# Performance work log

Measured on AMD Instinct MI355X. Metric: run time of the kernel, lower is better.

The kernel has to match this reference:

```python
import jax, jax.numpy as jnp
import numpy as np

B, L, DIN, D, H, NL, DFF = 4, 1024, 64, 512, 8, 3, 2048
DH = D // H
N_RBF = 8
LARGE_NEG, CLAMP = 10000.0, 20.0


def layernorm(x, g, b, eps=1e-5):
    m = x.mean(-1, keepdims=True)
    v = x.var(-1, keepdims=True)
    return (x - m) * jax.lax.rsqrt(v + eps) * g + b


def sinusoidal_pe(length, d):
    pos = np.arange(length, dtype=np.float32)[:, None]
    div = np.exp(np.arange(0, d, 2, dtype=np.float32) * (-np.log(10000.0) / d))
    pe = np.zeros((length, d), dtype=np.float32)
    pe[:, 0::2] = np.sin(pos * div)
    pe[:, 1::2] = np.cos(pos * div)
    return jnp.asarray(pe)


def rbf(v):
    centers = jnp.linspace(0.0, 1.0, N_RBF)
    widths = jnp.full((N_RBF,), 0.2)
    diff = (v[..., None] - centers) / (widths + 1e-6)
    return jnp.exp(-0.5 * diff * diff)


def setup_inputs() -> dict:
    key = jax.random.key(0)
    ks = jax.random.split(key, 40)
    g = lambda k, shape: (jax.random.normal(k, shape) * 0.02).astype(jnp.float32)
    feat_dim = D + 2 + 2 * N_RBF  # base PE + raw(2) + 2 RBFs
    inp = {
        "x": jax.random.normal(ks[0], (B, L, DIN), jnp.float32),
        "lengths": jax.random.randint(ks[1], (B,), L // 2, L + 1),
        "input_delay": jax.random.uniform(ks[2], (B,), jnp.float32),
        "c_local": jax.random.uniform(ks[3], (B, L), jnp.float32).at[:, 0].set(0.0),
        "c_sink": jax.random.uniform(ks[4], (B, L), jnp.float32),
        # input projection
        "in_w": g(ks[5], (D, DIN)), "in_b": jnp.zeros((D,)),
        # delay encoder: Linear(1,D) -> GELU -> Linear(D,D) -> LN
        "de_w1": g(ks[6], (D, 1)), "de_b1": jnp.zeros((D,)),
        "de_w2": g(ks[7], (D, D)), "de_b2": jnp.zeros((D,)),
        "de_ln_g": jnp.ones((D,)), "de_ln_b": jnp.zeros((D,)),
        # corr positional encoding
        "cpe_w": g(ks[8], (D, feat_dim)), "cpe_b": jnp.zeros((D,)),
        "cpe_ln_g": jnp.ones((D,)), "cpe_ln_b": jnp.zeros((D,)),
        "gain": jnp.float32(0.5),
        # bias params
        "alpha": jnp.float32(10.0), "beta": jnp.float32(10.0),
        "floor": jnp.float32(0.1), "gamma": jnp.float32(0.7),
        # per-layer stacks
        "inproj_w": g(ks[9], (NL, 3 * D, D)), "inproj_b": jnp.zeros((NL, 3 * D)),
        "outproj_w": g(ks[10], (NL, D, D)), "outproj_b": jnp.zeros((NL, D)),
        "ln1_g": jnp.ones((NL, D)), "ln1_b": jnp.zeros((NL, D)),
        "ln2_g": jnp.ones((NL, D)), "ln2_b": jnp.zeros((NL, D)),
        "ff_w1": g(ks[11], (NL, DFF, D)), "ff_b1": jnp.zeros((NL, DFF)),
        "ff_w2": g(ks[12], (NL, D, DFF)), "ff_b2": jnp.zeros((NL, D)),
        "out_ln_g": jnp.ones((D,)), "out_ln_b": jnp.zeros((D,)),
    }
    return inp


def _forward(x, input_delay, c_local, c_sink, in_w, in_b, de_w1, de_b1, de_w2, de_b2,
             de_ln_g, de_ln_b, cpe_w, cpe_b, cpe_ln_g, cpe_ln_b, gain, alpha, beta,
             floor, gamma, inproj_w, inproj_b, outproj_w, outproj_b, ln1_g, ln1_b,
             ln2_g, ln2_b, ff_w1, ff_b1, ff_w2, ff_b2, out_ln_g, out_ln_b, lengths):
    Bc, Lc, _ = x.shape
    mask = jnp.arange(Lc)[None, :] >= lengths[:, None]          # [B,L] True=pad

    # input projection
    h = x @ in_w.T + in_b

    # delay feature encoder
    e = input_delay[:, None] @ de_w1.T + de_b1
    e = jax.nn.gelu(e, approximate=False) @ de_w2.T + de_b2
    e = layernorm(e, de_ln_g, de_ln_b)
    h = h + e[:, None, :]

    # corr positional encoding (uses clamped correlations)
    cl = jnp.clip(c_local, 0.0, 1.0)
    cs = jnp.clip(c_sink, 0.0, 1.0)
    pe_base = jnp.broadcast_to(sinusoidal_pe(Lc, D)[None], (Bc, Lc, D))
    z = jnp.concatenate([pe_base, jnp.stack([cl, cs], -1), rbf(cl), rbf(cs)], axis=-1)
    pe = layernorm(z @ cpe_w.T + cpe_b, cpe_ln_g, cpe_ln_b)
    pe = gain * pe
    pe = jnp.where(mask[..., None], 0.0, pe)
    h = h + pe

    # neighbor-correlation attention bias [B,1,L,L] (identical across layers/heads)
    idx = jnp.arange(Lc)
    neigh = jnp.abs(idx[None, :] - idx[:, None]) == 1           # [L,L]
    c_edge = jnp.zeros((Bc, Lc, Lc), x.dtype)
    c_edge = c_edge.at[:, 1:, :-1].set(jnp.broadcast_to(c_local[:, 1:, None], (Bc, Lc - 1, Lc - 1)))
    c_edge = c_edge.at[:, :-1, 1:].set(jnp.broadcast_to(c_local[:, None, 1:], (Bc, Lc - 1, Lc - 1)))
    bias = alpha * jnp.where(neigh[None], c_edge, 0.0)
    bias = jnp.where(mask[:, :, None] | mask[:, None, :], 0.0, bias)

    # sink bias (row 0 only): floor + (1-floor)*(c_sink^gamma)
    c_remap = floor + (1.0 - floor) * jnp.power(cs + 1e-6, gamma)
    sink_row = beta * jnp.where(mask, 0.0, c_remap)             # [B,L]
    attn_bias = bias[:, None].at[:, :, 0, :].add(sink_row[:, None, :])  # [B,1,L,L]

    pad = mask[:, None, None, :].astype(x.dtype)                # [B,1,1,L]
    scale = 1.0 / (DH ** 0.5)

    for i in range(NL):
        hn = layernorm(h, ln1_g[i], ln1_b[i])
        qkv = hn @ inproj_w[i].T + inproj_b[i]                  # [B,L,3D]
        q, k, v = jnp.split(qkv, 3, axis=-1)
        q = q.reshape(Bc, Lc, H, DH).transpose(0, 2, 1, 3)      # [B,H,L,d]
        k = k.reshape(Bc, Lc, H, DH).transpose(0, 2, 1, 3)
        v = v.reshape(Bc, Lc, H, DH).transpose(0, 2, 1, 3)
        scores = jnp.einsum('bhqd,bhkd->bhqk', q, k) * scale + attn_bias
        scores = scores - LARGE_NEG * pad
        scores = scores - scores.max(axis=-1, keepdims=True)
        scores = jnp.clip(scores, -CLAMP, CLAMP)
        attn = jax.nn.softmax(scores, axis=-1)
        o = jnp.einsum('bhqk,bhkd->bhqd', attn, v)
        o = o.transpose(0, 2, 1, 3).reshape(Bc, Lc, D)
        h = h + (o @ outproj_w[i].T + outproj_b[i])
        hn2 = layernorm(h, ln2_g[i], ln2_b[i])
        ff = jax.nn.gelu(hn2 @ ff_w1[i].T + ff_b1[i], approximate=False)
        h = h + (ff @ ff_w2[i].T + ff_b2[i])

    return layernorm(h, out_ln_g, out_ln_b)


def reference(x, lengths, input_delay, c_local, c_sink, in_w, in_b, de_w1, de_b1,
              de_w2, de_b2, de_ln_g, de_ln_b, cpe_w, cpe_b, cpe_ln_g, cpe_ln_b, gain,
              alpha, beta, floor, gamma, inproj_w, inproj_b, outproj_w, outproj_b,
              ln1_g, ln1_b, ln2_g, ln2_b, ff_w1, ff_b1, ff_w2, ff_b2, out_ln_g, out_ln_b):
    return _forward(x, input_delay, c_local, c_sink, in_w, in_b, de_w1, de_b1, de_w2,
                    de_b2, de_ln_g, de_ln_b, cpe_w, cpe_b, cpe_ln_g, cpe_ln_b, gain,
                    alpha, beta, floor, gamma, inproj_w, inproj_b, outproj_w,
                    outproj_b, ln1_g, ln1_b, ln2_g, ln2_b, ff_w1, ff_b1, ff_w2, ff_b2,
                    out_ln_g, out_ln_b, lengths)
```

## Files before the change

### kernel.cpp

```cpp
#include <hip/hip_runtime.h>
#include <math.h>

#define BB 4
#define LL 1024
#define DIN 64
#define DD 512
#define HH 8
#define DH 64
#define NLAYER 3
#define DFF 2048
#define FEAT 530
#define FEATP 576
#define MM 4096

typedef float f32x4 __attribute__((ext_vector_type(4)));
typedef short s16x8 __attribute__((ext_vector_type(8)));

__device__ __forceinline__ unsigned short f2bf(float f) {
    unsigned int u = __float_as_uint(f);
    u += 0x7fffu + ((u >> 16) & 1u);
    return (unsigned short)(u >> 16);
}
__device__ __forceinline__ float bf2f(unsigned short u) {
    return __uint_as_float(((unsigned int)u) << 16);
}
__device__ __forceinline__ float gelu_exact(float x) {
    return 0.5f * x * (1.0f + erff(x * 0.7071067811865475f));
}
__device__ __forceinline__ float wave_reduce_sum(float v) {
    #pragma unroll
    for (int o = 32; o; o >>= 1) v += __shfl_down(v, o);
    return v;
}
__device__ __forceinline__ void gload16(const unsigned short* g, unsigned short* l) {
    __builtin_amdgcn_global_load_lds(
        (const __attribute__((address_space(1))) unsigned int*)g,
        (__attribute__((address_space(3))) unsigned int*)l, 16, 0, 0);
}

__global__ __launch_bounds__(256) void prep_kernel(
    const float* __restrict__ x, const float* __restrict__ inproj_w,
    const float* __restrict__ outproj_w, const float* __restrict__ ff_w1,
    const float* __restrict__ ff_w2, const float* __restrict__ in_w,
    const float* __restrict__ cpe_w,
    unsigned short* __restrict__ x_bf, unsigned short* __restrict__ w_inproj,
    unsigned short* __restrict__ w_outproj, unsigned short* __restrict__ w_ff1,
    unsigned short* __restrict__ w_ff2, unsigned short* __restrict__ w_in,
    unsigned short* __restrict__ w_cpe)
{
    const int N0 = MM * DIN;
    const int N1 = N0 + 3 * 1536 * 512;
    const int N2 = N1 + 3 * 512 * 512;
    const int N3 = N2 + 3 * 2048 * 512;
    const int N4 = N3 + 3 * 512 * 2048;
    const int N5 = N4 + 512 * 64;
    const int N6 = N5 + 512 * FEATP;
    for (int i = blockIdx.x * 256 + threadIdx.x; i < N6; i += gridDim.x * 256) {
        if (i < N0)      x_bf[i]          = f2bf(x[i]);
        else if (i < N1) w_inproj[i - N0] = f2bf(inproj_w[i - N0]);
        else if (i < N2) w_outproj[i - N1]= f2bf(outproj_w[i - N1]);
        else if (i < N3) w_ff1[i - N2]    = f2bf(ff_w1[i - N2]);
        else if (i < N4) w_ff2[i - N3]    = f2bf(ff_w2[i - N3]);
        else if (i < N5) w_in[i - N4]     = f2bf(in_w[i - N4]);
        else {
            int j = i - N5; int r = j / FEATP, c = j - r * FEATP;
            w_cpe[j] = (c < FEAT) ? f2bf(cpe_w[(size_t)r * FEAT + c]) : 0;
        }
    }
}

__global__ __launch_bounds__(256) void build_z_kernel(
    const float* __restrict__ c_local, const float* __restrict__ c_sink,
    const int* __restrict__ lengths,
    const float* __restrict__ beta_p, const float* __restrict__ floor_p,
    const float* __restrict__ gamma_p,
    unsigned short* __restrict__ Z, float* __restrict__ srow)
{
    int row = blockIdx.x;
    int b = row >> 10, l = row & 1023;
    int t = threadIdx.x;
    unsigned short* zr = Z + (size_t)row * FEATP;
    for (int d = t; d < DD; d += 256) {
        int i = d >> 1;
        float dv = expf((float)(2 * i) * (-0.017988946135618352f));
        float ang = (float)l * dv;
        zr[d] = f2bf((d & 1) ? cosf(ang) : sinf(ang));
    }
    if (t < 64) {
        float cl = c_local[(size_t)b * LL + l]; cl = fminf(fmaxf(cl, 0.f), 1.f);
        float cs = c_sink [(size_t)b * LL + l]; cs = fminf(fmaxf(cs, 0.f), 1.f);
        float v = 0.f;
        if (t == 0) v = cl;
        else if (t == 1) v = cs;
        else if (t < 10)  { float c = (float)(t - 2) * (1.0f / 7.0f);  float df = (cl - c) / 0.200001f; v = expf(-0.5f * df * df); }
        else if (t < 18)  { float c = (float)(t - 10) * (1.0f / 7.0f); float df = (cs - c) / 0.200001f; v = expf(-0.5f * df * df); }
        zr[512 + t] = (t < 18) ? f2bf(v) : 0;
        if (t == 32) {
            float sv = (*beta_p) * ((*floor_p) + (1.f - (*floor_p)) * powf(cs + 1e-6f, *gamma_p));
            srow[row] = (l < lengths[b]) ? sv : 0.f;
        }
    }
}

__global__ __launch_bounds__(512) void delay_kernel(
    const float* __restrict__ delay, const float* __restrict__ w1, const float* __restrict__ b1,
    const float* __restrict__ w2, const float* __restrict__ b2,
    const float* __restrict__ lng, const float* __restrict__ lnb,
    float* __restrict__ e)
{
    int b = blockIdx.x;
    int t = threadIdx.x;
    __shared__ float g1[DD];
    __shared__ float red[16];
    float t1 = delay[b] * w1[t] + b1[t];
    g1[t] = gelu_exact(t1);
    __syncthreads();
    const float* wr = w2 + (size_t)t * DD;
    float s = b2[t];
    for (int j = 0; j < DD; j += 4) {
        float4 w4 = *(const float4*)(wr + j);
        s += w4.x * g1[j] + w4.y * g1[j+1] + w4.z * g1[j+2] + w4.w * g1[j+3];
    }
    float rs = wave_reduce_sum(s);
    float rss = wave_reduce_sum(s * s);
    int lane = t & 63, w = t >> 6;
    if (lane == 0) { red[w] = rs; red[8 + w] = rss; }
    __syncthreads();
    float mean = 0.f, msq = 0.f;
    #pragma unroll
    for (int i = 0; i < 8; ++i) { mean += red[i]; msq += red[8 + i]; }
    mean *= (1.0f / DD); msq *= (1.0f / DD);
    float rstd = rsqrtf(msq - mean * mean + 1e-5f);
    e[(size_t)b * DD + t] = (s - mean) * rstd * lng[t] + lnb[t];
}

template<int BM, int BN, int FM, int FN, int WGN, int MODE>
__global__ __launch_bounds__(256) void gemm_t(
    const unsigned short* __restrict__ A, const unsigned short* __restrict__ W,
    const float* __restrict__ bias, const float* __restrict__ resid,
    float* __restrict__ outf, unsigned short* __restrict__ outb,
    int M, int N, int K)
{
    __shared__ __align__(16) unsigned short As[2][BM * 64];
    __shared__ __align__(16) unsigned short Ws[2][BN * 64];
    int bm = blockIdx.y * BM, bn = blockIdx.x * BN;
    int t = threadIdx.x;
    int lane = t & 63, wid = t >> 6;
    int wr = wid / WGN, wc = wid % WGN;
    int l15 = lane & 15, lg = lane >> 4;
    int sr = lane >> 3;
    int sc = ((lane & 7) ^ sr) * 8;
    int ph0 = (lg ^ (l15 & 7)) * 8;
    int ph1 = ((lg + 4) ^ (l15 & 7)) * 8;

    f32x4 acc[FM][FN] = {};
    int nk = K >> 6;

    auto stage = [&](int buf, int ks) {
        int kb = ks * 64;
        #pragma unroll
        for (int i = 0; i < BM / 32; ++i) {
            int row = wid * (BM / 4) + i * 8 + sr;
            gload16(A + (size_t)(bm + row) * K + kb + sc, &As[buf][(wid * (BM / 4) + i * 8) * 64]);
        }
        #pragma unroll
        for (int i = 0; i < BN / 32; ++i) {
            int row = wid * (BN / 4) + i * 8 + sr;
            gload16(W + (size_t)(bn + row) * K + kb + sc, &Ws[buf][(wid * (BN / 4) + i * 8) * 64]);
        }
    };

    stage(0, 0);
    __syncthreads();

    int cur = 0;
    for (int ks = 0; ks < nk; ++ks) {
        if (ks + 1 < nk) stage(cur ^ 1, ks + 1);
        s16x8 af0[FM], af1[FM], wf0[FN], wf1[FN];
        #pragma unroll
        for (int mi = 0; mi < FM; ++mi) {
            int row = wr * FM * 16 + mi * 16 + l15;
            af0[mi] = *(const s16x8*)&As[cur][row * 64 + ph0];
            af1[mi] = *(const s16x8*)&As[cur][row * 64 + ph1];
        }
        #pragma unroll
        for (int ni = 0; ni < FN; ++ni) {
            int row = wc * FN * 16 + ni * 16 + l15;
            wf0[ni] = *(const s16x8*)&Ws[cur][row * 64 + ph0];
            wf1[ni] = *(const s16x8*)&Ws[cur][row * 64 + ph1];
        }
        #pragma unroll
        for (int mi = 0; mi < FM; ++mi)
            #pragma unroll
            for (int ni = 0; ni < FN; ++ni) {
                acc[mi][ni] = __builtin_amdgcn_mfma_f32_16x16x32_bf16(af0[mi], wf0[ni], acc[mi][ni], 0, 0, 0);
                acc[mi][ni] = __builtin_amdgcn_mfma_f32_16x16x32_bf16(af1[mi], wf1[ni], acc[mi][ni], 0, 0, 0);
            }
        __syncthreads();
        cur ^= 1;
    }

    int rbase = (lane >> 4) * 4;
    #pragma unroll
    for (int mi = 0; mi < FM; ++mi) {
        #pragma unroll
        for (int ni = 0; ni < FN; ++ni) {
            int n = bn + wc * FN * 16 + ni * 16 + l15;
            float bzc = (MODE == 4) ? 0.f : bias[n];
            #pragma unroll
            for (int r2 = 0; r2 < 4; ++r2) {
                int m = bm + wr * FM * 16 + mi * 16 + rbase + r2;
                float v = acc[mi][ni][r2] + ((MODE == 4) ? bias[m] : bzc);
                size_t o = (size_t)m * N + n;
                if (MODE == 0)      outf[o] = v;
                else if (MODE == 1) outb[o] = f2bf(v);
                else if (MODE == 2) outf[o] = v + resid[o];
                else if (MODE == 3) outb[o] = f2bf(gelu_exact(v));
                else                outb[o] = f2bf(v);
            }
        }
    }
}

#define SK 72
#define SPB 72
__global__ __launch_bounds__(256) void attn_mfma(
    const unsigned short* __restrict__ qk, const unsigned short* __restrict__ Vt,
    const float* __restrict__ c_local, const float* __restrict__ srow,
    const int* __restrict__ lengths,
    const float* __restrict__ alpha_p,
    unsigned short* __restrict__ o)
{
    __shared__ __align__(16) unsigned short Ks[2][64 * SK];
    __shared__ __align__(16) unsigned short Vts[2][64 * SK];
    __shared__ __align__(16) unsigned short Psb[64 * SPB];

    int id = blockIdx.x;
    int q0 = (id & 15) * 64;
    int hh = (id >> 4) & 7;
    int b  = id >> 7;

    int t  = threadIdx.x;
    int lane = t & 63, w = t >> 6;
    int l15 = lane & 15, lg = lane >> 4;
    int len = lengths[b];
    int nt = (len + 63) >> 6;
    int kt0 = q0 >> 6;
    bool sink_blk = (q0 == 0);
    const float alpha = *alpha_p;

    const unsigned short* qrow = qk + (size_t)(b * LL + q0 + w * 16 + l15) * 1024 + hh * DH;
    s16x8 qf0 = *(const s16x8*)(qrow + lg * 8);
    s16x8 qf1 = *(const s16x8*)(qrow + 32 + lg * 8);
    #pragma unroll
    for (int j = 0; j < 8; ++j) {
        qf0[j] = (short)f2bf(bf2f((unsigned short)qf0[j]) * 0.125f);
        qf1[j] = (short)f2bf(bf2f((unsigned short)qf1[j]) * 0.125f);
    }

    float cm1[4], cp1[4];
    #pragma unroll
    for (int r2 = 0; r2 < 4; ++r2) {
        int qi = q0 + w * 16 + lg * 4 + r2;
        cm1[r2] = 0.f; cp1[r2] = 0.f;
        if (qi >= 1 && qi < len) {
            int src = (qi == 1 || qi == LL - 1) ? qi : qi - 1;
            cm1[r2] = alpha * c_local[(size_t)b * LL + src];
        }
        if (qi + 1 < LL && qi < len)
            cp1[r2] = alpha * c_local[(size_t)b * LL + qi + 1];
    }
    bool need_sink = (sink_blk && w == 0 && lg == 0);

    float m_run[4], l_run[4];
    f32x4 accO[4] = {};
    #pragma unroll
    for (int r2 = 0; r2 < 4; ++r2) { m_run[r2] = -1e30f; l_run[r2] = 0.f; }

    int sr = t >> 3, sc8 = (t & 7) * 8;
    const unsigned short* kbase = qk + (size_t)(b * LL) * 1024 + 512 + hh * DH;
    const unsigned short* vbase = Vt + (size_t)(hh * DH) * MM + b * LL;

    uint4 pk0 = *(const uint4*)(kbase + (size_t)sr * 1024 + sc8);
    uint4 pk1 = *(const uint4*)(kbase + (size_t)(sr + 32) * 1024 + sc8);
    uint4 pv0 = *(const uint4*)(vbase + (size_t)sr * MM + sc8);
    uint4 pv1 = *(const uint4*)(vbase + (size_t)(sr + 32) * MM + sc8);
    *(uint4*)&Ks[0][sr * SK + sc8]         = pk0;
    *(uint4*)&Ks[0][(sr + 32) * SK + sc8]  = pk1;
    *(uint4*)&Vts[0][sr * SK + sc8]        = pv0;
    *(uint4*)&Vts[0][(sr + 32) * SK + sc8] = pv1;
    __syncthreads();

    int cur = 0;
    for (int kt = 0; kt < nt; ++kt) {
        int k0 = kt * 64;
        bool pre = (kt + 1 < nt);
        if (pre) {
            int kn = k0 + 64;
            pk0 = *(const uint4*)(kbase + (size_t)(kn + sr) * 1024 + sc8);
            pk1 = *(const uint4*)(kbase + (size_t)(kn + sr + 32) * 1024 + sc8);
            pv0 = *(const uint4*)(vbase + (size_t)sr * MM + kn + sc8);
            pv1 = *(const uint4*)(vbase + (size_t)(sr + 32) * MM + kn + sc8);
        }

        f32x4 accS[4] = {};
        #pragma unroll
        for (int ct = 0; ct < 4; ++ct) {
            s16x8 kf0 = *(const s16x8*)&Ks[cur][(ct * 16 + l15) * SK + lg * 8];
            s16x8 kf1 = *(const s16x8*)&Ks[cur][(ct * 16 + l15) * SK + 32 + lg * 8];
            accS[ct] = __builtin_amdgcn_mfma_f32_16x16x32_bf16(qf0, kf0, accS[ct], 0, 0, 0);
            accS[ct] = __builtin_amdgcn_mfma_f32_16x16x32_bf16(qf1, kf1, accS[ct], 0, 0, 0);
        }

        float m4[4] = { -1e30f, -1e30f, -1e30f, -1e30f };
        bool slow = sink_blk || (kt >= kt0 - 1 && kt <= kt0 + 1) || (k0 + 64 > len);
        if (!slow) {
            #pragma unroll
            for (int ct = 0; ct < 4; ++ct)
                #pragma unroll
                for (int r2 = 0; r2 < 4; ++r2)
                    m4[r2] = fmaxf(m4[r2], accS[ct][r2]);
        } else if (k0 + 64 <= len) {
            #pragma unroll
            for (int ct = 0; ct < 4; ++ct) {
                int k = k0 + ct * 16 + l15;
                float sink_ct = need_sink ? srow[(size_t)b * LL + k] : 0.f;
                #pragma unroll
                for (int r2 = 0; r2 < 4; ++r2) {
                    int qi = q0 + w * 16 + lg * 4 + r2;
                    float v = accS[ct][r2];
                    if (k == qi - 1) v += cm1[r2];
                    else if (k == qi + 1) v += cp1[r2];
                    if (r2 == 0) v += sink_ct;
                    accS[ct][r2] = v;
                    m4[r2] = fmaxf(m4[r2], v);
                }
            }
        } else {
            #pragma unroll
            for (int ct = 0; ct < 4; ++ct) {
                int k = k0 + ct * 16 + l15;
                bool maskk = (k >= len);
                float sink_ct = need_sink ? srow[(size_t)b * LL + k] : 0.f;
                #pragma unroll
                for (int r2 = 0; r2 < 4; ++r2) {
                    int qi = q0 + w * 16 + lg * 4 + r2;
                    float v = accS[ct][r2];
                    if (k == qi - 1) v += cm1[r2];
                    else if (k == qi + 1 && !maskk) v += cp1[r2];
                    if (r2 == 0) v += sink_ct;
                    if (maskk) v -= 10000.f;
                    accS[ct][r2] = v;
                    m4[r2] = fmaxf(m4[r2], v);
                }
            }
        }

        #pragma unroll
        for (int r2 = 0; r2 < 4; ++r2) {
            #pragma unroll
            for (int msk = 1; msk < 16; msk <<= 1) m4[r2] = fmaxf(m4[r2], __shfl_xor(m4[r2], msk));
            float mnew = fmaxf(m_run[r2], m4[r2]);
            float scl = __expf(m_run[r2] - mnew);
            m_run[r2] = mnew;
            float rowsum = 0.f;
            #pragma unroll
            for (int ct = 0; ct < 4; ++ct) {
                float p = __expf(accS[ct][r2] - mnew);
                rowsum += p;
                Psb[(w * 16 + lg * 4 + r2) * SPB + ct * 16 + l15] = f2bf(p);
            }
            #pragma unroll
            for (int msk = 1; msk < 16; msk <<= 1) rowsum += __shfl_xor(rowsum, msk);
            l_run[r2] = l_run[r2] * scl + rowsum;
            #pragma unroll
            for (int dt = 0; dt < 4; ++dt) accO[dt][r2] *= scl;
        }

        #pragma unroll
        for (int kk = 0; kk < 2; ++kk) {
            s16x8 pf = *(const s16x8*)&Psb[(w * 16 + l15) * SPB + kk * 32 + lg * 8];
            #pragma unroll
            for (int dt = 0; dt < 4; ++dt) {
                s16x8 vf = *(const s16x8*)&Vts[cur][(dt * 16 + l15) * SK + kk * 32 + lg * 8];
                accO[dt] = __builtin_amdgcn_mfma_f32_16x16x32_bf16(pf, vf, accO[dt], 0, 0, 0);
            }
        }

        if (pre) {
            int nxt = cur ^ 1;
            *(uint4*)&Ks[nxt][sr * SK + sc8]         = pk0;
            *(uint4*)&Ks[nxt][(sr + 32) * SK + sc8]  = pk1;
            *(uint4*)&Vts[nxt][sr * SK + sc8]        = pv0;
            *(uint4*)&Vts[nxt][(sr + 32) * SK + sc8] = pv1;
        }
        __syncthreads();
        cur ^= 1;
    }

    #pragma unroll
    for (int r2 = 0; r2 < 4; ++r2) {
        float inv = 1.f / l_run[r2];
        int qi = q0 + w * 16 + lg * 4 + r2;
        #pragma unroll
        for (int dt = 0; dt < 4; ++dt)
            o[(size_t)(b * LL + qi) * DD + hh * DH + dt * 16 + l15] = f2bf(accO[dt][r2] * inv);
    }
}

__global__ __launch_bounds__(256) void embed_ep_kernel(
    const float* __restrict__ cpe_pre, const float* __restrict__ e,
    const int* __restrict__ lengths,
    const float* __restrict__ cpe_g, const float* __restrict__ cpe_lb,
    const float* __restrict__ gain_p, float* __restrict__ h)
{
    int row = blockIdx.x;
    int b = row >> 10, l = row & 1023;
    int t = threadIdx.x;
    __shared__ float red[16];
    const float* cp = cpe_pre + (size_t)row * DD;
    float v0 = cp[t], v1 = cp[t + 256];
    float s = v0 + v1, ss = v0 * v0 + v1 * v1;
    float rs = wave_reduce_sum(s), rss = wave_reduce_sum(ss);
    int lane = t & 63, w = t >> 6;
    if (lane == 0) { red[w] = rs; red[8 + w] = rss; }
    __syncthreads();
    float mean = 0.f, msq = 0.f;
    #pragma unroll
    for (int i = 0; i < 4; ++i) { mean += red[i]; msq += red[8 + i]; }
    mean *= (1.0f / DD); msq *= (1.0f / DD);
    float rstd = rsqrtf(msq - mean * mean + 1e-5f);
    bool maskp = (l >= lengths[b]);
    float gain = *gain_p;
    float pe0 = maskp ? 0.f : gain * ((v0 - mean) * rstd * cpe_g[t] + cpe_lb[t]);
    float pe1 = maskp ? 0.f : gain * ((v1 - mean) * rstd * cpe_g[t + 256] + cpe_lb[t + 256]);
    h[(size_t)row * DD + t]       += e[(size_t)b * DD + t] + pe0;
    h[(size_t)row * DD + t + 256] += e[(size_t)b * DD + t + 256] + pe1;
}

__global__ __launch_bounds__(256) void ln_kernel(
    const float* __restrict__ in, float* __restrict__ out,
    const float* __restrict__ g, const float* __restrict__ bta)
{
    int row = blockIdx.x; int t = threadIdx.x;
    __shared__ float red[16];
    const float* xr = in + (size_t)row * DD;
    float2 v = ((const float2*)xr)[t];
    float s = v.x + v.y, ss = v.x * v.x + v.y * v.y;
    float rs = wave_reduce_sum(s), rss = wave_reduce_sum(ss);
    int lane = t & 63, w = t >> 6;
    if (lane == 0) { red[w] = rs; red[8 + w] = rss; }
    __syncthreads();
    float mean = 0.f, msq = 0.f;
    #pragma unroll
    for (int i = 0; i < 4; ++i) { mean += red[i]; msq += red[8 + i]; }
    mean *= (1.0f / DD); msq *= (1.0f / DD);
    float rstd = rsqrtf(msq - mean * mean + 1e-5f);
    float2 gg = ((const float2*)g)[t], bb = ((const float2*)bta)[t];
    float2 o;
    o.x = (v.x - mean) * rstd * gg.x + bb.x;
    o.y = (v.y - mean) * rstd * gg.y + bb.y;
    ((float2*)(out + (size_t)row * DD))[t] = o;
}

__global__ __launch_bounds__(256) void ln_bf16_kernel(
    const float* __restrict__ in, unsigned short* __restrict__ out,
    const float* __restrict__ g, const float* __restrict__ bta)
{
    int row = blockIdx.x; int t = threadIdx.x;
    __shared__ float red[16];
    const float* xr = in + (size_t)row * DD;
    float2 v = ((const float2*)xr)[t];
    float s = v.x + v.y, ss = v.x * v.x + v.y * v.y;
    float rs = wave_reduce_sum(s), rss = wave_reduce_sum(ss);
    int lane = t & 63, w = t >> 6;
    if (lane == 0) { red[w] = rs; red[8 + w] = rss; }
    __syncthreads();
    float mean = 0.f, msq = 0.f;
    #pragma unroll
    for (int i = 0; i < 4; ++i) { mean += red[i]; msq += red[8 + i]; }
    mean *= (1.0f / DD); msq *= (1.0f / DD);
    float rstd = rsqrtf(msq - mean * mean + 1e-5f);
    float2 gg = ((const float2*)g)[t], bb = ((const float2*)bta)[t];
    ushort2 o;
    o.x = f2bf((v.x - mean) * rstd * gg.x + bb.x);
    o.y = f2bf((v.y - mean) * rstd * gg.y + bb.y);
    ((ushort2*)(out + (size_t)row * DD))[t] = o;
}

extern "C" void kernel_launch(void* const* d_in, const int* in_sizes, int n_in,
                              void* d_out, int out_size, void* d_ws, size_t ws_size,
                              hipStream_t stream)
{
    const float* x          = (const float*)d_in[0];
    const int*   lengths    = (const int*)  d_in[1];
    const float* input_delay= (const float*)d_in[2];
    const float* c_local    = (const float*)d_in[3];
    const float* c_sink     = (const float*)d_in[4];
    const float* in_w       = (const float*)d_in[5];
    const float* in_b       = (const float*)d_in[6];
    const float* de_w1      = (const float*)d_in[7];
    const float* de_b1      = (const float*)d_in[8];
    const float* de_w2      = (const float*)d_in[9];
    const float* de_b2      = (const float*)d_in[10];
    const float* de_ln_g    = (const float*)d_in[11];
    const float* de_ln_b    = (const float*)d_in[12];
    const float* cpe_w      = (const float*)d_in[13];
    const float* cpe_b      = (const float*)d_in[14];
    const float* cpe_ln_g   = (const float*)d_in[15];
    const float* cpe_ln_b   = (const float*)d_in[16];
    const float* gain       = (const float*)d_in[17];
    const float* alpha      = (const float*)d_in[18];
    const float* beta       = (const float*)d_in[19];
    const float* floorp     = (const float*)d_in[20];
    const float* gammap     = (const float*)d_in[21];
    const float* inproj_w   = (const float*)d_in[22];
    const float* inproj_b   = (const float*)d_in[23];
    const float* outproj_w  = (const float*)d_in[24];
    const float* outproj_b  = (const float*)d_in[25];
    const float* ln1_g      = (const float*)d_in[26];
    const float* ln1_b      = (const float*)d_in[27];
    const float* ln2_g      = (const float*)d_in[28];
    const float* ln2_b      = (const float*)d_in[29];
    const float* ff_w1      = (const float*)d_in[30];
    const float* ff_b1      = (const float*)d_in[31];
    const float* ff_w2      = (const float*)d_in[32];
    const float* ff_b2      = (const float*)d_in[33];
    const float* out_ln_g   = (const float*)d_in[34];
    const float* out_ln_b   = (const float*)d_in[35];

    char* base = (char*)d_ws;
    float* h            = (float*)base;
    unsigned short* act1 = (unsigned short*)(base + 8u*1024*1024);
    char* bigb          = base + 12u*1024*1024;
    unsigned short* qkb  = (unsigned short*)bigb;
    unsigned short* vtb  = (unsigned short*)(bigb + 12u*1024*1024);
    unsigned short* ffb  = (unsigned short*)bigb;
    unsigned short* Zb   = (unsigned short*)bigb;
    unsigned short* x_bf = (unsigned short*)(bigb + 5u*1024*1024);
    float* cpe_pre       = (float*)(bigb + 8u*1024*1024);
    unsigned short* w_inproj  = (unsigned short*)(base + 28u*1024*1024);
    unsigned short* w_outproj = w_inproj  + (size_t)3*1536*512;
    unsigned short* w_ff1     = w_outproj + (size_t)3*512*512;
    unsigned short* w_ff2     = w_ff1     + (size_t)3*2048*512;
    unsigned short* w_in      = w_ff2     + (size_t)3*512*2048;
    unsigned short* w_cpe     = w_in      + (size_t)512*64;
    float* e                  = (float*)(w_cpe + (size_t)512*FEATP);
    float* srow               = e + (size_t)BB*DD;

    prep_kernel<<<2048, 256, 0, stream>>>(x, inproj_w, outproj_w, ff_w1, ff_w2, in_w, cpe_w,
                                          x_bf, w_inproj, w_outproj, w_ff1, w_ff2, w_in, w_cpe);
    delay_kernel<<<BB, 512, 0, stream>>>(input_delay, de_w1, de_b1, de_w2, de_b2, de_ln_g, de_ln_b, e);
    build_z_kernel<<<MM, 256, 0, stream>>>(c_local, c_sink, lengths, beta, floorp, gammap, Zb, srow);

    gemm_t<64, 64, 2, 2, 2, 0><<<dim3(DD / 64, MM / 64), 256, 0, stream>>>(
        x_bf, w_in, in_b, nullptr, h, nullptr, MM, DD, DIN);
    gemm_t<64, 64, 2, 2, 2, 0><<<dim3(DD / 64, MM / 64), 256, 0, stream>>>(
        Zb, w_cpe, cpe_b, nullptr, cpe_pre, nullptr, MM, DD, FEATP);
    embed_ep_kernel<<<MM, 256, 0, stream>>>(cpe_pre, e, lengths, cpe_ln_g, cpe_ln_b, gain, h);

    for (int i = 0; i < NLAYER; ++i) {
        const unsigned short* wqk = w_inproj + (size_t)i * 1536 * 512;
        const unsigned short* wv  = wqk + (size_t)1024 * 512;
        ln_bf16_kernel<<<MM, 256, 0, stream>>>(h, act1, ln1_g + (size_t)i * DD, ln1_b + (size_t)i * DD);
        gemm_t<64, 128, 2, 4, 2, 1><<<dim3(1024 / 128, MM / 64), 256, 0, stream>>>(
            act1, wqk, inproj_b + (size_t)i * 1536, nullptr, nullptr, qkb, MM, 1024, DD);
        gemm_t<64, 64, 2, 2, 2, 4><<<dim3(MM / 64, DD / 64), 256, 0, stream>>>(
            wv, act1, inproj_b + (size_t)i * 1536 + 1024, nullptr, nullptr, vtb, DD, MM, DD);
        attn_mfma<<<512, 256, 0, stream>>>(qkb, vtb, c_local, srow, lengths, alpha, act1);
        gemm_t<64, 64, 2, 2, 2, 2><<<dim3(DD / 64, MM / 64), 256, 0, stream>>>(
            act1, w_outproj + (size_t)i * 512 * 512, outproj_b + (size_t)i * DD,
            h, h, nullptr, MM, DD, DD);
        ln_bf16_kernel<<<MM, 256, 0, stream>>>(h, act1, ln2_g + (size_t)i * DD, ln2_b + (size_t)i * DD);
        gemm_t<128, 128, 4, 4, 2, 3><<<dim3(DFF / 128, MM / 128), 256, 0, stream>>>(
            act1, w_ff1 + (size_t)i * 2048 * 512, ff_b1 + (size_t)i * DFF,
            nullptr, nullptr, ffb, MM, DFF, DD);
        gemm_t<64, 64, 2, 2, 2, 2><<<dim3(DD / 64, MM / 64), 256, 0, stream>>>(
            ffb, w_ff2 + (size_t)i * 512 * 2048, ff_b2 + (size_t)i * DD,
            h, h, nullptr, MM, DD, DFF);
    }
    ln_kernel<<<MM, 256, 0, stream>>>(h, (float*)d_out, out_ln_g, out_ln_b);
}
```

Measured before the change: 440.4 us.

## Halve attention query tile to 32 rows with 2 waves and single-buffered K/V

Attention blocks now handle 32 queries with 128 threads, doubling the grid to 1024 blocks to improve CU occupancy and load balance. The K/V shared tiles become single-buffered, with register prefetch of the next tile and a barrier before compute, reducing LDS use per block. The trade-off is twice the K/V tile traffic per query and less overlap of LDS stores with compute.

New measurement: 592.7 us. 1.35x slower.

```diff
diff --git a/kernel.cpp b/kernel.cpp
--- a/kernel.cpp
+++ b/kernel.cpp
@@ -224,28 +224,29 @@
 
 #define SK 72
 #define SPB 72
-__global__ __launch_bounds__(256) void attn_mfma(
+__global__ __launch_bounds__(128) void attn_mfma(
     const unsigned short* __restrict__ qk, const unsigned short* __restrict__ Vt,
     const float* __restrict__ c_local, const float* __restrict__ srow,
     const int* __restrict__ lengths,
     const float* __restrict__ alpha_p,
     unsigned short* __restrict__ o)
 {
-    __shared__ __align__(16) unsigned short Ks[2][64 * SK];
-    __shared__ __align__(16) unsigned short Vts[2][64 * SK];
-    __shared__ __align__(16) unsigned short Psb[64 * SPB];
+    __shared__ __align__(16) unsigned short Ks[64 * SK];
+    __shared__ __align__(16) unsigned short Vts[64 * SK];
+    __shared__ __align__(16) unsigned short Psb[32 * SPB];
 
     int id = blockIdx.x;
-    int q0 = (id & 15) * 64;
-    int hh = (id >> 4) & 7;
-    int b  = id >> 7;
+    int q0 = (id & 31) * 32;
+    int hh = (id >> 5) & 7;
+    int b  = id >> 8;
 
     int t  = threadIdx.x;
     int lane = t & 63, w = t >> 6;
     int l15 = lane & 15, lg = lane >> 4;
     int len = lengths[b];
     int nt = (len + 63) >> 6;
-    int kt0 = q0 >> 6;
+    int ktlo = (q0 > 0 ? q0 - 1 : 0) >> 6;
+    int kthi = (q0 + 32) >> 6;
     bool sink_blk = (q0 == 0);
     const float alpha = *alpha_p;
 
@@ -281,39 +282,41 @@
     const unsigned short* kbase = qk + (size_t)(b * LL) * 1024 + 512 + hh * DH;
     const unsigned short* vbase = Vt + (size_t)(hh * DH) * MM + b * LL;
 
-    uint4 pk0 = *(const uint4*)(kbase + (size_t)sr * 1024 + sc8);
-    uint4 pk1 = *(const uint4*)(kbase + (size_t)(sr + 32) * 1024 + sc8);
-    uint4 pv0 = *(const uint4*)(vbase + (size_t)sr * MM + sc8);
-    uint4 pv1 = *(const uint4*)(vbase + (size_t)(sr + 32) * MM + sc8);
-    *(uint4*)&Ks[0][sr * SK + sc8]         = pk0;
-    *(uint4*)&Ks[0][(sr + 32) * SK + sc8]  = pk1;
-    *(uint4*)&Vts[0][sr * SK + sc8]        = pv0;
-    *(uint4*)&Vts[0][(sr + 32) * SK + sc8] = pv1;
-    __syncthreads();
-
-    int cur = 0;
+    uint4 pk[4], pv[4];
+    #pragma unroll
+    for (int u = 0; u < 4; ++u) {
+        pk[u] = *(const uint4*)(kbase + (size_t)(sr + u * 16) * 1024 + sc8);
+        pv[u] = *(const uint4*)(vbase + (size_t)(sr + u * 16) * MM + sc8);
+    }
+
     for (int kt = 0; kt < nt; ++kt) {
         int k0 = kt * 64;
-        bool pre = (kt + 1 < nt);
-        if (pre) {
+        #pragma unroll
+        for (int u = 0; u < 4; ++u) {
+            *(uint4*)&Ks[(sr + u * 16) * SK + sc8]  = pk[u];
+            *(uint4*)&Vts[(sr + u * 16) * SK + sc8] = pv[u];
+        }
+        if (kt + 1 < nt) {
             int kn = k0 + 64;
-            pk0 = *(const uint4*)(kbase + (size_t)(kn + sr) * 1024 + sc8);
-            pk1 = *(const uint4*)(kbase + (size_t)(kn + sr + 32) * 1024 + sc8);
-            pv0 = *(const uint4*)(vbase + (size_t)sr * MM + kn + sc8);
-            pv1 = *(const uint4*)(vbase + (size_t)(sr + 32) * MM + kn + sc8);
-        }
+            #pragma unroll
+            for (int u = 0; u < 4; ++u) {
+                pk[u] = *(const uint4*)(kbase + (size_t)(kn + sr + u * 16) * 1024 + sc8);
+                pv[u] = *(const uint4*)(vbase + (size_t)(sr + u * 16) * MM + kn + sc8);
+            }
+        }
+        __syncthreads();
 
         f32x4 accS[4] = {};
         #pragma unroll
         for (int ct = 0; ct < 4; ++ct) {
-            s16x8 kf0 = *(const s16x8*)&Ks[cur][(ct * 16 + l15) * SK + lg * 8];
-            s16x8 kf1 = *(const s16x8*)&Ks[cur][(ct * 16 + l15) * SK + 32 + lg * 8];
+            s16x8 kf0 = *(const s16x8*)&Ks[(ct * 16 + l15) * SK + lg * 8];
+            s16x8 kf1 = *(const s16x8*)&Ks[(ct * 16 + l15) * SK + 32 + lg * 8];
             accS[ct] = __builtin_amdgcn_mfma_f32_16x16x32_bf16(qf0, kf0, accS[ct], 0, 0, 0);
             accS[ct] = __builtin_amdgcn_mfma_f32_16x16x32_bf16(qf1, kf1, accS[ct], 0, 0, 0);
         }
 
         float m4[4] = { -1e30f, -1e30f, -1e30f, -1e30f };
-        bool slow = sink_blk || (kt >= kt0 - 1 && kt <= kt0 + 1) || (k0 + 64 > len);
+        bool slow = sink_blk || (kt >= ktlo && kt <= kthi) || (k0 + 64 > len);
         if (!slow) {
             #pragma unroll
             for (int ct = 0; ct < 4; ++ct)
@@ -382,20 +385,11 @@
             s16x8 pf = *(const s16x8*)&Psb[(w * 16 + l15) * SPB + kk * 32 + lg * 8];
             #pragma unroll
             for (int dt = 0; dt < 4; ++dt) {
-                s16x8 vf = *(const s16x8*)&Vts[cur][(dt * 16 + l15) * SK + kk * 32 + lg * 8];
+                s16x8 vf = *(const s16x8*)&Vts[(dt * 16 + l15) * SK + kk * 32 + lg * 8];
                 accO[dt] = __builtin_amdgcn_mfma_f32_16x16x32_bf16(pf, vf, accO[dt], 0, 0, 0);
             }
         }
-
-        if (pre) {
-            int nxt = cur ^ 1;
-            *(uint4*)&Ks[nxt][sr * SK + sc8]         = pk0;
-            *(uint4*)&Ks[nxt][(sr + 32) * SK + sc8]  = pk1;
-            *(uint4*)&Vts[nxt][sr * SK + sc8]        = pv0;
-            *(uint4*)&Vts[nxt][(sr + 32) * SK + sc8] = pv1;
-        }
         __syncthreads();
-        cur ^= 1;
     }
 
     #pragma unroll
@@ -567,7 +561,7 @@
             act1, wqk, inproj_b + (size_t)i * 1536, nullptr, nullptr, qkb, MM, 1024, DD);
         gemm_t<64, 64, 2, 2, 2, 4><<<dim3(MM / 64, DD / 64), 256, 0, stream>>>(
             wv, act1, inproj_b + (size_t)i * 1536 + 1024, nullptr, nullptr, vtb, DD, MM, DD);
-        attn_mfma<<<512, 256, 0, stream>>>(qkb, vtb, c_local, srow, lengths, alpha, act1);
+        attn_mfma<<<1024, 128, 0, stream>>>(qkb, vtb, c_local, srow, lengths, alpha, act1);
         gemm_t<64, 64, 2, 2, 2, 2><<<dim3(DD / 64, MM / 64), 256, 0, stream>>>(
             act1, w_outproj + (size_t)i * 512 * 512, outproj_b + (size_t)i * DD,
             h, h, nullptr, MM, DD, DD);
```
